# Kernel tuning notes

Hardware: AMD Instinct MI355X
Metric: run time of the kernel (lower is better)

## Reference

```python
import jax, jax.numpy as jnp
import numpy as np

N_EMBD = 1024
N_HEAD = 16
HEAD_DIM = N_EMBD // N_HEAD
B, T, I = 8, 1024, 257


def _ln(x, g, b, eps=1e-5):
    mu = jnp.mean(x, axis=-1, keepdims=True)
    var = jnp.var(x, axis=-1, keepdims=True)
    return (x - mu) * jax.lax.rsqrt(var + eps) * g + b


def setup_inputs() -> dict:
    key = jax.random.key(0)
    ks = jax.random.split(key, 16)
    s = 0.02
    d = {
        "x": jax.random.normal(ks[0], (B, T, N_EMBD), jnp.float32),
        "encoder_output": jax.random.normal(ks[1], (B, I, N_EMBD), jnp.float32),
        # LayerNorm params
        "ln1_g": jnp.ones((N_EMBD,), jnp.float32), "ln1_b": jnp.zeros((N_EMBD,), jnp.float32),
        "ln2_g": jnp.ones((N_EMBD,), jnp.float32), "ln2_b": jnp.zeros((N_EMBD,), jnp.float32),
        "ln3_g": jnp.ones((N_EMBD,), jnp.float32), "ln3_b": jnp.zeros((N_EMBD,), jnp.float32),
        # self-attention
        "w_qkv": jax.random.normal(ks[2], (N_EMBD, 3 * N_EMBD), jnp.float32) * s,
        "b_qkv": jnp.zeros((3 * N_EMBD,), jnp.float32),
        "w_ao": jax.random.normal(ks[3], (N_EMBD, N_EMBD), jnp.float32) * s,
        "b_ao": jnp.zeros((N_EMBD,), jnp.float32),
        # cross-attention
        "w_q": jax.random.normal(ks[4], (N_EMBD, N_EMBD), jnp.float32) * s,
        "b_q": jnp.zeros((N_EMBD,), jnp.float32),
        "w_kv": jax.random.normal(ks[5], (N_EMBD, 2 * N_EMBD), jnp.float32) * s,
        "b_kv": jnp.zeros((2 * N_EMBD,), jnp.float32),
        "w_co": jax.random.normal(ks[6], (N_EMBD, N_EMBD), jnp.float32) * s,
        "b_co": jnp.zeros((N_EMBD,), jnp.float32),
        # MLP
        "w_fc": jax.random.normal(ks[7], (N_EMBD, 4 * N_EMBD), jnp.float32) * s,
        "b_fc": jnp.zeros((4 * N_EMBD,), jnp.float32),
        "w_mo": jax.random.normal(ks[8], (4 * N_EMBD, N_EMBD), jnp.float32) * s,
        "b_mo": jnp.zeros((N_EMBD,), jnp.float32),
    }
    return d


def _heads(t, L):
    # [B, L, C] -> [B, H, L, D]
    return t.reshape(B, L, N_HEAD, HEAD_DIM).transpose(0, 2, 1, 3)


def _self_attn(x, w_qkv, b_qkv, w_ao, b_ao):
    qkv = x @ w_qkv + b_qkv
    q, k, v = jnp.split(qkv, 3, axis=-1)
    q, k, v = _heads(q, T), _heads(k, T), _heads(v, T)
    att = jnp.einsum('bhtd,bhsd->bhts', q, k) * (1.0 / np.sqrt(HEAD_DIM))
    causal = jnp.tril(jnp.ones((T, T), bool))
    att = jnp.where(causal, att, -jnp.inf)
    att = jax.nn.softmax(att, axis=-1)
    out = jnp.einsum('bhts,bhsd->bhtd', att, v).transpose(0, 2, 1, 3).reshape(B, T, N_EMBD)
    return out @ w_ao + b_ao


def _cross_attn(x, enc, w_q, b_q, w_kv, b_kv, w_co, b_co):
    q = _heads(x @ w_q + b_q, T)
    kv = enc @ w_kv + b_kv
    k, v = jnp.split(kv, 2, axis=-1)
    k, v = _heads(k, I), _heads(v, I)
    att = jnp.einsum('bhtd,bhid->bhti', q, k) * (1.0 / np.sqrt(HEAD_DIM))
    att = jax.nn.softmax(att, axis=-1)
    out = jnp.einsum('bhti,bhid->bhtd', att, v).transpose(0, 2, 1, 3).reshape(B, T, N_EMBD)
    return out @ w_co + b_co


def reference(x, encoder_output, ln1_g, ln1_b, ln2_g, ln2_b, ln3_g, ln3_b,
              w_qkv, b_qkv, w_ao, b_ao, w_q, b_q, w_kv, b_kv, w_co, b_co,
              w_fc, b_fc, w_mo, b_mo):
    x = x + _self_attn(_ln(x, ln1_g, ln1_b), w_qkv, b_qkv, w_ao, b_ao)
    x = x + _cross_attn(_ln(x, ln2_g, ln2_b), encoder_output, w_q, b_q, w_kv, b_kv, w_co, b_co)
    h = _ln(x, ln3_g, ln3_b)
    h = jax.nn.gelu(h @ w_fc + b_fc, approximate=True)  # GELU tanh approximation
    x = x + h @ w_mo + b_mo
    return x
```

## Files before the change

kernel.cpp:

```cpp
#include <hip/hip_runtime.h>
#include <hip/hip_bf16.h>

#define N_EMBD 1024
#define N_HEAD 16
#define HEAD_DIM 64
#define BATCH 8
#define SEQ_T 1024
#define SEQ_I 257

typedef __attribute__((ext_vector_type(8))) short short8_t;
typedef __attribute__((ext_vector_type(4))) float f32x4;

union U8 { uint4 u; short8_t s; };

static __device__ __forceinline__ unsigned short f2b(float f)
{
    unsigned int u = __float_as_uint(f);
    u = (u + 0x7fffu + ((u >> 16) & 1u)) >> 16;
    return (unsigned short)u;
}

__device__ __forceinline__ float gelu_tanh(float u)
{
    float z = 0.7978845608028654f * (u + 0.044715f * u * u * u);
    z = fmaxf(z, -15.0f);
    const float e = __expf(-2.0f * z);
    const float t = (1.0f - e) / (1.0f + e);
    return 0.5f * u * (1.0f + t);
}

__global__ __launch_bounds__(256)
void wcast_t(const float* __restrict__ W, short* __restrict__ WT, int K, int N)
{
    __shared__ float t[32][33];
    const int n0 = blockIdx.x * 32, k0 = blockIdx.y * 32;
    const int c = threadIdx.x & 31, r4 = (threadIdx.x >> 5) * 4;
    #pragma unroll
    for (int i = 0; i < 4; ++i)
        t[r4 + i][c] = W[(size_t)(k0 + r4 + i) * N + n0 + c];
    __syncthreads();
    #pragma unroll
    for (int i = 0; i < 4; ++i)
        WT[(size_t)(n0 + r4 + i) * K + k0 + c] = (short)f2b(t[c][r4 + i]);
}

__global__ __launch_bounds__(256)
void cast_bf16(const float* __restrict__ in, short* __restrict__ out)
{
    const int i = blockIdx.x * 256 + threadIdx.x;
    const float4 v = ((const float4*)in)[i];
    unsigned int w0 = (unsigned int)f2b(v.x) | ((unsigned int)f2b(v.y) << 16);
    unsigned int w1 = (unsigned int)f2b(v.z) | ((unsigned int)f2b(v.w) << 16);
    ((uint2*)out)[i] = make_uint2(w0, w1);
}

__global__ __launch_bounds__(256)
void ln_bf16(const float* __restrict__ in, const float* __restrict__ gamma,
             const float* __restrict__ beta, short* __restrict__ out)
{
    const int row = blockIdx.x;
    const int tid = threadIdx.x;
    const float4 v = *(const float4*)(in + (size_t)row * N_EMBD + tid * 4);
    float s  = v.x + v.y + v.z + v.w;
    float ss = v.x*v.x + v.y*v.y + v.z*v.z + v.w*v.w;
    #pragma unroll
    for (int off = 32; off >= 1; off >>= 1) {
        s  += __shfl_down(s,  off);
        ss += __shfl_down(ss, off);
    }
    __shared__ float rs[4], rss[4];
    const int wid = tid >> 6, lane = tid & 63;
    if (lane == 0) { rs[wid] = s; rss[wid] = ss; }
    __syncthreads();
    s  = rs[0] + rs[1] + rs[2] + rs[3];
    ss = rss[0] + rss[1] + rss[2] + rss[3];
    const float mean = s * (1.0f / N_EMBD);
    const float var  = ss * (1.0f / N_EMBD) - mean * mean;
    const float rstd = rsqrtf(var + 1e-5f);
    const float4 g = *(const float4*)(gamma + tid * 4);
    const float4 b = *(const float4*)(beta  + tid * 4);
    float o0 = (v.x - mean) * rstd * g.x + b.x;
    float o1 = (v.y - mean) * rstd * g.y + b.y;
    float o2 = (v.z - mean) * rstd * g.z + b.z;
    float o3 = (v.w - mean) * rstd * g.w + b.w;
    unsigned int w0 = (unsigned int)f2b(o0) | ((unsigned int)f2b(o1) << 16);
    unsigned int w1 = (unsigned int)f2b(o2) | ((unsigned int)f2b(o3) << 16);
    ((uint2*)(out + (size_t)row * N_EMBD))[tid] = make_uint2(w0, w1);
}

template<int EPI>
__global__ __launch_bounds__(256, 2)
void gemm_mfma(const short* __restrict__ A, const short* __restrict__ WT,
               const float* __restrict__ bias, const float* __restrict__ res,
               void* __restrict__ outv, int M, int N, int K, int lda, int gnx)
{
    __shared__ short As[2][128 * 64];
    __shared__ short Bs[2][128 * 64];
    const int tid  = threadIdx.x;

    const int nwg = gridDim.x;
    const int lin = (blockIdx.x & 7) * (nwg >> 3) + (blockIdx.x >> 3);
    const int bm  = (lin / gnx) * 128;
    const int bn  = (lin % gnx) * 128;

    const int lane = tid & 63;
    const int wid  = tid >> 6;
    const int wr   = (wid >> 1) * 64;
    const int wc   = (wid & 1) * 64;
    const int fr   = lane & 15;
    const int kg   = lane >> 4;

    const int r_ = tid >> 3;
    const int g_ = (tid & 7) ^ (r_ & 7);
    const int dstbase = (tid & ~63) * 16;

    #define STAGE(buf, k0)                                                          \
        _Pragma("unroll")                                                           \
        for (int p = 0; p < 4; ++p) {                                               \
            const int rowA = min(bm + p * 32 + r_, M - 1);                          \
            __builtin_amdgcn_global_load_lds(                                       \
                (const __attribute__((address_space(1))) void*)                     \
                    (A + (size_t)rowA * lda + (k0) + g_ * 8),                       \
                (__attribute__((address_space(3))) void*)                           \
                    ((char*)As[buf] + p * 4096 + dstbase), 16, 0, 0);               \
            const int rowB = bn + p * 32 + r_;                                      \
            __builtin_amdgcn_global_load_lds(                                       \
                (const __attribute__((address_space(1))) void*)                     \
                    (WT + (size_t)rowB * K + (k0) + g_ * 8),                        \
                (__attribute__((address_space(3))) void*)                           \
                    ((char*)Bs[buf] + p * 4096 + dstbase), 16, 0, 0);               \
        }

    f32x4 acc[4][4];
    #pragma unroll
    for (int i = 0; i < 4; ++i)
        #pragma unroll
        for (int j = 0; j < 4; ++j)
            acc[i][j] = (f32x4){0.f, 0.f, 0.f, 0.f};

    STAGE(0, 0);
    __syncthreads();

    const int nkt = K >> 6;
    for (int kt = 0; kt < nkt; ++kt) {
        const int cur = kt & 1;
        if (kt + 1 < nkt) { STAGE(cur ^ 1, (kt + 1) << 6); }

        const short* AsC = As[cur];
        const short* BsC = Bs[cur];
        #pragma unroll
        for (int kk = 0; kk < 2; ++kk) {
            short8_t af[4], bf[4];
            #pragma unroll
            for (int f = 0; f < 4; ++f) {
                const int ra = wr + f * 16 + fr;
                af[f] = *(const short8_t*)(AsC + ra * 64 + (((kk * 4 + kg) ^ (ra & 7)) * 8));
                const int rb = wc + f * 16 + fr;
                bf[f] = *(const short8_t*)(BsC + rb * 64 + (((kk * 4 + kg) ^ (rb & 7)) * 8));
            }
            #pragma unroll
            for (int i = 0; i < 4; ++i)
                #pragma unroll
                for (int j = 0; j < 4; ++j)
                    acc[i][j] = __builtin_amdgcn_mfma_f32_16x16x32_bf16(af[i], bf[j], acc[i][j], 0, 0, 0);
        }
        __syncthreads();
    }
    #undef STAGE

    #pragma unroll
    for (int i = 0; i < 4; ++i) {
        #pragma unroll
        for (int r = 0; r < 4; ++r) {
            const int m = bm + wr + i * 16 + kg * 4 + r;
            if (m >= M) continue;
            #pragma unroll
            for (int j = 0; j < 4; ++j) {
                const int n = bn + wc + j * 16 + fr;
                float v = acc[i][j][r] + bias[n];
                if (EPI == 1) v += res[(size_t)m * N + n];
                if (EPI == 2) v = gelu_tanh(v);
                if (EPI == 1) ((float*)outv)[(size_t)m * N + n] = v;
                else          ((short*)outv)[(size_t)m * N + n] = (short)f2b(v);
            }
        }
    }
}

template<bool CAUSAL>
__global__ __launch_bounds__(256, 2)
void attn_mfma(const short* __restrict__ Qm, const short* __restrict__ Km,
               const short* __restrict__ Vm, short* __restrict__ out,
               int qStride, int kStride, int kRows)
{
    __shared__ short Ks[32 * 64];
    __shared__ unsigned int VtU[36 * 32];
    __shared__ unsigned int PA[4][320];

    const int tid  = threadIdx.x;
    const int lane = tid & 63;
    const int wid  = tid >> 6;
    const int bid  = blockIdx.x;
    const int qt   = CAUSAL ? (15 - (bid >> 7)) : (bid >> 7);
    const int bh   = bid & 127;
    const int b    = bh >> 4, h = bh & 15;
    const int qb   = qt * 64;
    const int fr   = lane & 15;
    const int g    = lane >> 4;

    const int qrow = qb + wid * 16 + fr;
    const short* qptr = Qm + (size_t)(b * SEQ_T + qrow) * qStride + h * HEAD_DIM + g * 8;
    U8 qf0, qf1;
    qf0.u = *(const uint4*)(qptr);
    qf1.u = *(const uint4*)(qptr + 32);

    f32x4 accO[4];
    #pragma unroll
    for (int i = 0; i < 4; ++i) accO[i] = (f32x4){0.f, 0.f, 0.f, 0.f};
    float mrun = -1e30f, lrun = 0.f;

    const int ntiles = CAUSAL ? (2 * qt + 2) : ((kRows + 31) >> 5);
    const size_t kbase = (size_t)b * kRows;

    for (int it = 0; it < ntiles; ++it) {
        const int kb = it * 32;
        __syncthreads();

        {
            const int krow  = min(kb + (tid >> 3), kRows - 1);
            const int gslot = (tid & 7) ^ ((tid >> 3) & 7);
            __builtin_amdgcn_global_load_lds(
                (const __attribute__((address_space(1))) void*)
                    (Km + (kbase + krow) * (size_t)kStride + h * HEAD_DIM + gslot * 8),
                (__attribute__((address_space(3))) void*)((char*)Ks + tid * 16), 16, 0, 0);
        }
        #pragma unroll
        for (int v = 0; v < 2; ++v) {
            const int idx = v * 256 + tid;
            const int d2 = idx & 31, kp = idx >> 5;
            const int kr0 = min(kb + 2 * kp,     kRows - 1);
            const int kr1 = min(kb + 2 * kp + 1, kRows - 1);
            const unsigned int u0 = *(const unsigned int*)
                (Vm + (kbase + kr0) * (size_t)kStride + h * HEAD_DIM + 2 * d2);
            const unsigned int u1 = *(const unsigned int*)
                (Vm + (kbase + kr1) * (size_t)kStride + h * HEAD_DIM + 2 * d2);
            VtU[36 * d2 + kp]      = (u0 & 0xffffu) | (u1 << 16);
            VtU[36 * d2 + 18 + kp] = (u0 >> 16)    | (u1 & 0xffff0000u);
        }
        __syncthreads();

        f32x4 s0 = (f32x4){0.f,0.f,0.f,0.f}, s1 = (f32x4){0.f,0.f,0.f,0.f};
        {
            const uint4* K4 = (const uint4*)Ks;
            U8 ka;
            ka.u = K4[8 * fr        + ((g)     ^ (fr & 7))];
            s0 = __builtin_amdgcn_mfma_f32_16x16x32_bf16(ka.s, qf0.s, s0, 0, 0, 0);
            ka.u = K4[8 * fr        + ((4 + g) ^ (fr & 7))];
            s0 = __builtin_amdgcn_mfma_f32_16x16x32_bf16(ka.s, qf1.s, s0, 0, 0, 0);
            ka.u = K4[8 * (16 + fr) + ((g)     ^ (fr & 7))];
            s1 = __builtin_amdgcn_mfma_f32_16x16x32_bf16(ka.s, qf0.s, s1, 0, 0, 0);
            ka.u = K4[8 * (16 + fr) + ((4 + g) ^ (fr & 7))];
            s1 = __builtin_amdgcn_mfma_f32_16x16x32_bf16(ka.s, qf1.s, s1, 0, 0, 0);
        }

        float sv[8];
        #pragma unroll
        for (int r = 0; r < 4; ++r) {
            sv[r]     = s0[r] * 0.125f;
            sv[4 + r] = s1[r] * 0.125f;
            const int k0 = kb + 4 * g + r;
            const int k1 = k0 + 16;
            if (CAUSAL ? (k0 > qrow) : (k0 >= kRows)) sv[r]     = -1e30f;
            if (CAUSAL ? (k1 > qrow) : (k1 >= kRows)) sv[4 + r] = -1e30f;
        }
        float tm = sv[0];
        #pragma unroll
        for (int j = 1; j < 8; ++j) tm = fmaxf(tm, sv[j]);
        tm = fmaxf(tm, __shfl_xor(tm, 16));
        tm = fmaxf(tm, __shfl_xor(tm, 32));
        const float newm = fmaxf(mrun, tm);
        const float fs = __expf(mrun - newm);
        mrun = newm;
        float p[8], ps = 0.f;
        #pragma unroll
        for (int j = 0; j < 8; ++j) { p[j] = __expf(sv[j] - newm); ps += p[j]; }
        ps += __shfl_xor(ps, 16);
        ps += __shfl_xor(ps, 32);
        lrun = lrun * fs + ps;

        float frr[4];
        #pragma unroll
        for (int r = 0; r < 4; ++r) frr[r] = __shfl(fs, 4 * g + r);
        #pragma unroll
        for (int db = 0; db < 4; ++db)
            #pragma unroll
            for (int r = 0; r < 4; ++r) accO[db][r] *= frr[r];

        {
            uint2* paw = (uint2*)PA[wid];
            paw[10 * fr + g] = make_uint2(
                (unsigned int)f2b(p[0]) | ((unsigned int)f2b(p[1]) << 16),
                (unsigned int)f2b(p[2]) | ((unsigned int)f2b(p[3]) << 16));
            paw[10 * fr + 4 + g] = make_uint2(
                (unsigned int)f2b(p[4]) | ((unsigned int)f2b(p[5]) << 16),
                (unsigned int)f2b(p[6]) | ((unsigned int)f2b(p[7]) << 16));
        }
        U8 pf;
        pf.u = ((const uint4*)PA[wid])[5 * fr + g];

        #pragma unroll
        for (int db = 0; db < 4; ++db) {
            const int d = db * 16 + fr;
            const uint2 v0 = ((const uint2*)VtU)[9 * d + 2 * g];
            const uint2 v1 = ((const uint2*)VtU)[9 * d + 2 * g + 1];
            U8 vf; vf.u = make_uint4(v0.x, v0.y, v1.x, v1.y);
            accO[db] = __builtin_amdgcn_mfma_f32_16x16x32_bf16(pf.s, vf.s, accO[db], 0, 0, 0);
        }
    }

    float lr[4];
    #pragma unroll
    for (int r = 0; r < 4; ++r) lr[r] = 1.0f / __shfl(lrun, 4 * g + r);
    #pragma unroll
    for (int db = 0; db < 4; ++db) {
        #pragma unroll
        for (int r = 0; r < 4; ++r) {
            const int row = qb + wid * 16 + 4 * g + r;
            const int col = h * HEAD_DIM + db * 16 + fr;
            out[(size_t)(b * SEQ_T + row) * N_EMBD + col] = (short)f2b(accO[db][r] * lr[r]);
        }
    }
}

extern "C" void kernel_launch(void* const* d_in, const int* in_sizes, int n_in,
                              void* d_out, int out_size, void* d_ws, size_t ws_size,
                              hipStream_t stream)
{
    const float* x     = (const float*)d_in[0];
    const float* enc   = (const float*)d_in[1];
    const float* ln1_g = (const float*)d_in[2];
    const float* ln1_b = (const float*)d_in[3];
    const float* ln2_g = (const float*)d_in[4];
    const float* ln2_b = (const float*)d_in[5];
    const float* ln3_g = (const float*)d_in[6];
    const float* ln3_b = (const float*)d_in[7];
    const float* w_qkv = (const float*)d_in[8];
    const float* b_qkv = (const float*)d_in[9];
    const float* w_ao  = (const float*)d_in[10];
    const float* b_ao  = (const float*)d_in[11];
    const float* w_q   = (const float*)d_in[12];
    const float* b_q   = (const float*)d_in[13];
    const float* w_kv  = (const float*)d_in[14];
    const float* b_kv  = (const float*)d_in[15];
    const float* w_co  = (const float*)d_in[16];
    const float* b_co  = (const float*)d_in[17];
    const float* w_fc  = (const float*)d_in[18];
    const float* b_fc  = (const float*)d_in[19];
    const float* w_mo  = (const float*)d_in[20];
    const float* b_mo  = (const float*)d_in[21];
    float* outp = (float*)d_out;

    short* wt_qkv = (short*)d_ws;
    short* wt_ao  = wt_qkv + 3145728;
    short* wt_q   = wt_ao  + 1048576;
    short* wt_kv  = wt_q   + 1048576;
    short* wt_co  = wt_kv  + 2097152;
    short* wt_fc  = wt_co  + 1048576;
    short* wt_mo  = wt_fc  + 4194304;
    short* enc_b  = wt_mo  + 4194304;
    short* y_b    = enc_b  + 2105344;
    short* qkv_b  = y_b    + 8388608;
    short* h_b    = qkv_b;
    short* attn_b = qkv_b  + 33554432;
    short* q_b    = attn_b + 8388608;
    float* x1     = (float*)(q_b + 8388608);
    float* x2     = x1 + 8388608;
    short* kv_b   = (short*)(x2 + 8388608);

    const int ROWS  = BATCH * SEQ_T;
    const int EROWS = BATCH * SEQ_I;

    wcast_t<<<dim3(3072/32, 1024/32), 256, 0, stream>>>(w_qkv, wt_qkv, 1024, 3072);
    wcast_t<<<dim3(1024/32, 1024/32), 256, 0, stream>>>(w_ao,  wt_ao,  1024, 1024);
    wcast_t<<<dim3(1024/32, 1024/32), 256, 0, stream>>>(w_q,   wt_q,   1024, 1024);
    wcast_t<<<dim3(2048/32, 1024/32), 256, 0, stream>>>(w_kv,  wt_kv,  1024, 2048);
    wcast_t<<<dim3(1024/32, 1024/32), 256, 0, stream>>>(w_co,  wt_co,  1024, 1024);
    wcast_t<<<dim3(4096/32, 1024/32), 256, 0, stream>>>(w_fc,  wt_fc,  1024, 4096);
    wcast_t<<<dim3(1024/32, 4096/32), 256, 0, stream>>>(w_mo,  wt_mo,  4096, 1024);
    cast_bf16<<<2056, 256, 0, stream>>>(enc, enc_b);

    ln_bf16<<<ROWS, 256, 0, stream>>>(x, ln1_g, ln1_b, y_b);
    gemm_mfma<0><<<1536, 256, 0, stream>>>(
        y_b, wt_qkv, b_qkv, nullptr, qkv_b, ROWS, 3072, 1024, 1024, 24);
    attn_mfma<true><<<2048, 256, 0, stream>>>(
        qkv_b, qkv_b + 1024, qkv_b + 2048, attn_b, 3072, 3072, SEQ_T);
    gemm_mfma<1><<<512, 256, 0, stream>>>(
        attn_b, wt_ao, b_ao, x, x1, ROWS, 1024, 1024, 1024, 8);
    ln_bf16<<<ROWS, 256, 0, stream>>>(x1, ln2_g, ln2_b, y_b);
    gemm_mfma<0><<<512, 256, 0, stream>>>(
        y_b, wt_q, b_q, nullptr, q_b, ROWS, 1024, 1024, 1024, 8);
    gemm_mfma<0><<<272, 256, 0, stream>>>(
        enc_b, wt_kv, b_kv, nullptr, kv_b, EROWS, 2048, 1024, 1024, 16);
    attn_mfma<false><<<2048, 256, 0, stream>>>(
        q_b, kv_b, kv_b + 1024, attn_b, 1024, 2048, SEQ_I);
    gemm_mfma<1><<<512, 256, 0, stream>>>(
        attn_b, wt_co, b_co, x1, x2, ROWS, 1024, 1024, 1024, 8);
    ln_bf16<<<ROWS, 256, 0, stream>>>(x2, ln3_g, ln3_b, y_b);
    gemm_mfma<2><<<2048, 256, 0, stream>>>(
        y_b, wt_fc, b_fc, nullptr, h_b, ROWS, 4096, 1024, 1024, 32);
    gemm_mfma<1><<<512, 256, 0, stream>>>(
        h_b, wt_mo, b_mo, x2, outp, ROWS, 1024, 4096, 4096, 8);
}
```

Measured before the change: 672.1 us.

## Triple-buffer GEMM with BK=32, vmcnt-based waits, and XCD-aware tile mapping

The GEMM K tile drops from 64 to 32 and LDS goes from two buffers to three, so loads run two stages ahead. The full __syncthreads is replaced by a partial s_waitcnt vmcnt plus a raw barrier. Launch bounds rise to 3 blocks per CU, and a new mpc parameter places contiguous M-tiles on the same XCD so they share weight tiles in L2. The risks are more barriers per K step, since each step does half the MFMA work, and the hand-counted vmcnt must match exactly or the pipeline reads stale data.

```diff
diff --git a/kernel.cpp b/kernel.cpp
--- a/kernel.cpp
+++ b/kernel.cpp
@@ -89,19 +89,25 @@
 }
 
 template<int EPI>
-__global__ __launch_bounds__(256, 2)
+__global__ __launch_bounds__(256, 3)
 void gemm_mfma(const short* __restrict__ A, const short* __restrict__ WT,
                const float* __restrict__ bias, const float* __restrict__ res,
-               void* __restrict__ outv, int M, int N, int K, int lda, int gnx)
-{
-    __shared__ short As[2][128 * 64];
-    __shared__ short Bs[2][128 * 64];
-    const int tid  = threadIdx.x;
+               void* __restrict__ outv, int M, int N, int K, int lda,
+               int gnx, int mpc)
+{
+    __shared__ short As[3][128 * 32];
+    __shared__ short Bs[3][128 * 32];
+    const int tid = threadIdx.x;
 
     const int nwg = gridDim.x;
-    const int lin = (blockIdx.x & 7) * (nwg >> 3) + (blockIdx.x >> 3);
-    const int bm  = (lin / gnx) * 128;
-    const int bn  = (lin % gnx) * 128;
+    const int cs  = nwg >> 3;
+    const int xcd = blockIdx.x & 7;
+    const int loc = blockIdx.x >> 3;
+    int bmi, bni;
+    if (mpc > 1) { bmi = xcd * mpc + (loc % mpc); bni = loc / mpc; }
+    else { const int lin = xcd * cs + loc; bmi = lin / gnx; bni = lin % gnx; }
+    const int bm = bmi * 128;
+    const int bn = bni * 128;
 
     const int lane = tid & 63;
     const int wid  = tid >> 6;
@@ -110,25 +116,37 @@
     const int fr   = lane & 15;
     const int kg   = lane >> 4;
 
-    const int r_ = tid >> 3;
-    const int g_ = (tid & 7) ^ (r_ & 7);
-    const int dstbase = (tid & ~63) * 16;
-
-    #define STAGE(buf, k0)                                                          \
-        _Pragma("unroll")                                                           \
-        for (int p = 0; p < 4; ++p) {                                               \
-            const int rowA = min(bm + p * 32 + r_, M - 1);                          \
-            __builtin_amdgcn_global_load_lds(                                       \
-                (const __attribute__((address_space(1))) void*)                     \
-                    (A + (size_t)rowA * lda + (k0) + g_ * 8),                       \
-                (__attribute__((address_space(3))) void*)                           \
-                    ((char*)As[buf] + p * 4096 + dstbase), 16, 0, 0);               \
-            const int rowB = bn + p * 32 + r_;                                      \
-            __builtin_amdgcn_global_load_lds(                                       \
-                (const __attribute__((address_space(1))) void*)                     \
-                    (WT + (size_t)rowB * K + (k0) + g_ * 8),                        \
-                (__attribute__((address_space(3))) void*)                           \
-                    ((char*)Bs[buf] + p * 4096 + dstbase), 16, 0, 0);               \
+    const int r0_ = tid >> 2;
+    const int r1_ = (256 + tid) >> 2;
+    const int g0_ = (tid & 3) ^ (r0_ & 3);
+    const int g1_ = (tid & 3) ^ (r1_ & 3);
+    const int dst0 = (tid & ~63) * 16;
+    const int dst1 = 4096 + (tid & ~63) * 16;
+
+    #define STAGE(buf, k0)                                                      \
+        {                                                                       \
+            const int rowA0 = min(bm + r0_, M - 1);                             \
+            const int rowA1 = min(bm + r1_, M - 1);                             \
+            __builtin_amdgcn_global_load_lds(                                   \
+                (const __attribute__((address_space(1))) void*)                 \
+                    (A + (size_t)rowA0 * lda + (k0) + g0_ * 8),                 \
+                (__attribute__((address_space(3))) void*)                       \
+                    ((char*)As[buf] + dst0), 16, 0, 0);                         \
+            __builtin_amdgcn_global_load_lds(                                   \
+                (const __attribute__((address_space(1))) void*)                 \
+                    (A + (size_t)rowA1 * lda + (k0) + g1_ * 8),                 \
+                (__attribute__((address_space(3))) void*)                       \
+                    ((char*)As[buf] + dst1), 16, 0, 0);                         \
+            __builtin_amdgcn_global_load_lds(                                   \
+                (const __attribute__((address_space(1))) void*)                 \
+                    (WT + (size_t)(bn + r0_) * K + (k0) + g0_ * 8),             \
+                (__attribute__((address_space(3))) void*)                       \
+                    ((char*)Bs[buf] + dst0), 16, 0, 0);                         \
+            __builtin_amdgcn_global_load_lds(                                   \
+                (const __attribute__((address_space(1))) void*)                 \
+                    (WT + (size_t)(bn + r1_) * K + (k0) + g1_ * 8),             \
+                (__attribute__((address_space(3))) void*)                       \
+                    ((char*)Bs[buf] + dst1), 16, 0, 0);                         \
         }
 
     f32x4 acc[4][4];
@@ -139,32 +157,37 @@
             acc[i][j] = (f32x4){0.f, 0.f, 0.f, 0.f};
 
     STAGE(0, 0);
-    __syncthreads();
-
-    const int nkt = K >> 6;
-    for (int kt = 0; kt < nkt; ++kt) {
-        const int cur = kt & 1;
-        if (kt + 1 < nkt) { STAGE(cur ^ 1, (kt + 1) << 6); }
-
-        const short* AsC = As[cur];
-        const short* BsC = Bs[cur];
-        #pragma unroll
-        for (int kk = 0; kk < 2; ++kk) {
-            short8_t af[4], bf[4];
+    STAGE(1, 32);
+    asm volatile("s_waitcnt vmcnt(4)" ::: "memory");
+    __builtin_amdgcn_s_barrier();
+    __builtin_amdgcn_sched_barrier(0);
+
+    const int nkt = K >> 5;
+    int bc = 0, bs = 2;
+    for (int t = 0; t < nkt; ++t) {
+        if (t + 2 < nkt) STAGE(bs, (t + 2) << 5);
+
+        const short* AsC = As[bc];
+        const short* BsC = Bs[bc];
+        short8_t af[4], bf[4];
+        #pragma unroll
+        for (int f = 0; f < 4; ++f) {
+            const int ra = wr + f * 16 + fr;
+            af[f] = *(const short8_t*)(AsC + ra * 32 + ((kg ^ (ra & 3)) * 8));
+            const int rb = wc + f * 16 + fr;
+            bf[f] = *(const short8_t*)(BsC + rb * 32 + ((kg ^ (rb & 3)) * 8));
+        }
+        #pragma unroll
+        for (int i = 0; i < 4; ++i)
             #pragma unroll
-            for (int f = 0; f < 4; ++f) {
-                const int ra = wr + f * 16 + fr;
-                af[f] = *(const short8_t*)(AsC + ra * 64 + (((kk * 4 + kg) ^ (ra & 7)) * 8));
-                const int rb = wc + f * 16 + fr;
-                bf[f] = *(const short8_t*)(BsC + rb * 64 + (((kk * 4 + kg) ^ (rb & 7)) * 8));
-            }
-            #pragma unroll
-            for (int i = 0; i < 4; ++i)
-                #pragma unroll
-                for (int j = 0; j < 4; ++j)
-                    acc[i][j] = __builtin_amdgcn_mfma_f32_16x16x32_bf16(af[i], bf[j], acc[i][j], 0, 0, 0);
-        }
-        __syncthreads();
+            for (int j = 0; j < 4; ++j)
+                acc[i][j] = __builtin_amdgcn_mfma_f32_16x16x32_bf16(af[i], bf[j], acc[i][j], 0, 0, 0);
+
+        asm volatile("s_waitcnt vmcnt(4)" ::: "memory");
+        __builtin_amdgcn_s_barrier();
+        __builtin_amdgcn_sched_barrier(0);
+        bc = (bc == 2) ? 0 : bc + 1;
+        bs = (bs == 2) ? 0 : bs + 1;
     }
     #undef STAGE
 
@@ -391,23 +414,23 @@
 
     ln_bf16<<<ROWS, 256, 0, stream>>>(x, ln1_g, ln1_b, y_b);
     gemm_mfma<0><<<1536, 256, 0, stream>>>(
-        y_b, wt_qkv, b_qkv, nullptr, qkv_b, ROWS, 3072, 1024, 1024, 24);
+        y_b, wt_qkv, b_qkv, nullptr, qkv_b, ROWS, 3072, 1024, 1024, 24, 8);
     attn_mfma<true><<<2048, 256, 0, stream>>>(
         qkv_b, qkv_b + 1024, qkv_b + 2048, attn_b, 3072, 3072, SEQ_T);
     gemm_mfma<1><<<512, 256, 0, stream>>>(
-        attn_b, wt_ao, b_ao, x, x1, ROWS, 1024, 1024, 1024, 8);
+        attn_b, wt_ao, b_ao, x, x1, ROWS, 1024, 1024, 1024, 8, 8);
     ln_bf16<<<ROWS, 256, 0, stream>>>(x1, ln2_g, ln2_b, y_b);
     gemm_mfma<0><<<512, 256, 0, stream>>>(
-        y_b, wt_q, b_q, nullptr, q_b, ROWS, 1024, 1024, 1024, 8);
+        y_b, wt_q, b_q, nullptr, q_b, ROWS, 1024, 1024, 1024, 8, 8);
     gemm_mfma<0><<<272, 256, 0, stream>>>(
-        enc_b, wt_kv, b_kv, nullptr, kv_b, EROWS, 2048, 1024, 1024, 16);
+        enc_b, wt_kv, b_kv, nullptr, kv_b, EROWS, 2048, 1024, 1024, 16, 1);
     attn_mfma<false><<<2048, 256, 0, stream>>>(
         q_b, kv_b, kv_b + 1024, attn_b, 1024, 2048, SEQ_I);
     gemm_mfma<1><<<512, 256, 0, stream>>>(
-        attn_b, wt_co, b_co, x1, x2, ROWS, 1024, 1024, 1024, 8);
+        attn_b, wt_co, b_co, x1, x2, ROWS, 1024, 1024, 1024, 8, 8);
     ln_bf16<<<ROWS, 256, 0, stream>>>(x2, ln3_g, ln3_b, y_b);
     gemm_mfma<2><<<2048, 256, 0, stream>>>(
-        y_b, wt_fc, b_fc, nullptr, h_b, ROWS, 4096, 1024, 1024, 32);
+        y_b, wt_fc, b_fc, nullptr, h_b, ROWS, 4096, 1024, 1024, 32, 8);
     gemm_mfma<1><<<512, 256, 0, stream>>>(
-        h_b, wt_mo, b_mo, x2, outp, ROWS, 1024, 4096, 4096, 8);
-}
+        h_b, wt_mo, b_mo, x2, outp, ROWS, 1024, 4096, 4096, 8, 8);
+}
```

Result: slower. 712.8 us (+6.1%).
